# Performance work log

Measured on AMD Instinct MI355X. Metric: run time of the kernel, lower is better.

Reference implementation:

```python
import jax, jax.numpy as jnp
import numpy as np

N = 100000      # nodes
E = 1600000     # edges (avg degree 16)
D_IN = 128
D_OUT = 64
N_SCALES = 3
DEPTH = 10
TELEPORTS = np.array([0.1, 0.2, 0.3], dtype=np.float32)


def setup_inputs() -> dict:
    key = jax.random.key(0)
    ks = jax.random.split(key, 9)
    data = jax.random.normal(ks[0], (N, D_IN), dtype=jnp.float32)
    src = jax.random.randint(ks[1], (E,), 0, N, dtype=jnp.int32)
    tgt = jax.random.randint(ks[2], (E,), 0, N, dtype=jnp.int32)
    s = 1.0 / np.sqrt(D_IN)
    Ws = jax.random.uniform(ks[3], (N_SCALES, D_IN, D_OUT), jnp.float32, -s, s)
    bs = jax.random.uniform(ks[4], (N_SCALES, D_OUT), jnp.float32, -s, s)
    W_src = jax.random.uniform(ks[5], (D_IN, D_OUT), jnp.float32, -s, s)
    b_src = jax.random.uniform(ks[6], (D_OUT,), jnp.float32, -s, s)
    so = 1.0 / np.sqrt(D_OUT)
    W_tgt = jax.random.uniform(ks[7], (D_OUT, D_OUT), jnp.float32, -so, so)
    b_tgt = jax.random.uniform(ks[8], (D_OUT,), jnp.float32, -so, so)
    return {"data": data, "src": src, "tgt": tgt, "Ws": Ws, "bs": bs,
            "W_src": W_src, "b_src": b_src, "W_tgt": W_tgt, "b_tgt": b_tgt}


def reference(data, src, tgt, Ws, bs, W_src, b_src, W_tgt, b_tgt):
    # per-target-node degree (indices.unique counts repeated per edge)
    deg = jax.ops.segment_sum(jnp.ones((E,), jnp.float32), tgt, num_segments=N)
    deg_inv = 1.0 / jnp.maximum(deg, 1.0)           # [N]
    edge_w = deg_inv[tgt][:, None]                  # [E,1] normalized factor

    def laplacian(x):                               # x: [N, D_OUT]
        diff = (x[tgt] - x[src]) * edge_w           # (own - source_message)/deg
        return jax.ops.segment_sum(diff, tgt, num_segments=N)

    lap3 = jax.vmap(laplacian)                      # over scale dim

    t = jnp.asarray(TELEPORTS)[:, None, None]       # [S,1,1]
    emb = jnp.einsum('nd,sdo->sno', data, Ws) + bs[:, None, :]   # [S,N,O]
    out = emb
    for _ in range(DEPTH):
        out = (1.0 - t) * lap3(out) + t * emb
    scales = jax.nn.relu(out)                       # [S,N,O]

    s_att = data @ W_src + b_src                    # [N,O]
    t_att = jnp.einsum('sno,op->snp', scales, W_tgt) + b_tgt     # [S,N,O]
    logits = jnp.einsum('snp,np->sn', t_att, s_att)              # [S,N]
    att = jax.nn.softmax(logits, axis=0)            # softmax over scales
    return jnp.einsum('sn,sno->no', att, scales)    # [N,O]
```

## Files before the change

kernel.cpp:

```cpp
#include <hip/hip_runtime.h>
#include <hip/hip_bf16.h>

#define NN   100000
#define EE   1600000
#define CAP  48
#define NT   6250
#define NPB  192
#define NB   521

typedef __attribute__((ext_vector_type(8))) short bf16x8;
typedef __attribute__((ext_vector_type(4))) float f32x4;

__device__ inline short f2b_rne(float f) {
  union { float f; unsigned u; } x; x.f = f;
  unsigned r = x.u + 0x7fffu + ((x.u >> 16) & 1u);
  return (short)(r >> 16);
}
__device__ inline unsigned pack_rne(float lo, float hi) {
  unsigned ul = __float_as_uint(lo); ul += 0x7fffu + ((ul >> 16) & 1u);
  unsigned uh = __float_as_uint(hi); uh += 0x7fffu + ((uh >> 16) & 1u);
  return __builtin_amdgcn_perm(uh, ul, 0x07060302u);
}
__device__ inline float lo2f(unsigned u) { return __uint_as_float(u << 16); }
__device__ inline float hi2f(unsigned u) { return __uint_as_float(u & 0xffff0000u); }

__global__ __launch_bounds__(256) void k_fillA(const int* __restrict__ tgt,
                                               int* __restrict__ ghist) {
  __shared__ int h[NB];
  for (int i = threadIdx.x; i < NB; i += 256) h[i] = 0;
  __syncthreads();
  int e = blockIdx.x * 4096 + threadIdx.x;
#pragma unroll
  for (int k = 0; k < 16; ++k, e += 256)
    if (e < EE) atomicAdd(&h[tgt[e] / NPB], 1);
  __syncthreads();
  for (int i = threadIdx.x; i < NB; i += 256)
    if (h[i]) atomicAdd(&ghist[i], h[i]);
}

__global__ __launch_bounds__(256) void k_scan(const int* __restrict__ ghist,
                                              int* __restrict__ base,
                                              int* __restrict__ tail) {
  __shared__ int v[1024];
  const int tid = threadIdx.x;
  for (int i = tid; i < 1024; i += 256) v[i] = (i < NB) ? ghist[i] : 0;
  __syncthreads();
  for (int off = 1; off < 1024; off <<= 1) {
    int tmp[4];
#pragma unroll
    for (int j = 0; j < 4; ++j) {
      int i = tid + j * 256;
      tmp[j] = (i >= off) ? v[i - off] : 0;
    }
    __syncthreads();
#pragma unroll
    for (int j = 0; j < 4; ++j) v[tid + j * 256] += tmp[j];
    __syncthreads();
  }
  for (int i = tid; i <= NB; i += 256) {
    int bb = (i == 0) ? 0 : v[i - 1];
    base[i] = bb;
    if (i < NB) tail[i] = bb;
  }
}

__global__ __launch_bounds__(256) void k_fillB(const int* __restrict__ tgt,
                                               const int* __restrict__ src,
                                               int* tail, uint2* __restrict__ part) {
  __shared__ int hist[NB], cur[NB], basel[NB];
  const int tid = threadIdx.x;
  for (int i = tid; i < NB; i += 256) { hist[i] = 0; cur[i] = 0; }
  __syncthreads();
  const int e0 = blockIdx.x * 4096 + tid;
  int tv[16], sv[16];
#pragma unroll
  for (int k = 0; k < 16; ++k) {
    int e = e0 + k * 256;
    tv[k] = -1;
    if (e < EE) {
      tv[k] = tgt[e]; sv[k] = src[e];
      atomicAdd(&hist[tv[k] / NPB], 1);
    }
  }
  __syncthreads();
  for (int b = tid; b < NB; b += 256)
    if (hist[b]) basel[b] = atomicAdd(&tail[b], hist[b]);
  __syncthreads();
#pragma unroll
  for (int k = 0; k < 16; ++k) {
    if (tv[k] >= 0) {
      int b = tv[k] / NPB;
      int r = atomicAdd(&cur[b], 1);
      part[basel[b] + r] = make_uint2((unsigned)sv[k], (unsigned)tv[k]);
    }
  }
}

__global__ __launch_bounds__(256) void k_fillC(const int* __restrict__ base,
                                               const uint2* __restrict__ part,
                                               int* __restrict__ cnt,
                                               int* __restrict__ col) {
  __shared__ int ccnt[NPB];
  __shared__ int ccol[NPB * CAP];
  const int b = blockIdx.x, tid = threadIdx.x;
  for (int i = tid; i < NPB; i += 256) ccnt[i] = 0;
  __syncthreads();
  const int lo = base[b], hi = base[b + 1];
  for (int i = lo + tid; i < hi; i += 256) {
    uint2 e = part[i];
    int nl = (int)e.y - b * NPB;
    int p = atomicAdd(&ccnt[nl], 1);
    if (p < CAP) ccol[nl * CAP + p] = (int)e.x;
  }
  __syncthreads();
  const int n0 = b * NPB;
  for (int i = tid; i < NPB; i += 256)
    if (n0 + i < NN) cnt[n0 + i] = ccnt[i];
  for (int i = tid; i < NPB * CAP; i += 256) {
    int n = n0 + i / CAP;
    if (n < NN) col[(size_t)n0 * CAP + i] = ccol[i];
  }
}

__global__ void k_cast(const float* __restrict__ data, unsigned* __restrict__ y0) {
  int i = blockIdx.x * 256 + threadIdx.x;
  const float2 v = ((const float2*)data)[i];
  y0[i] = pack_rne(v.x, v.y);
}

template <int MODE>
__global__ __launch_bounds__(256) void k_prop(
    const int* __restrict__ cnt, const int* __restrict__ col,
    const unsigned* __restrict__ xin, unsigned* xout,
    const unsigned* s0p, const unsigned* s1p,
    unsigned* __restrict__ z0, unsigned* __restrict__ z1,
    unsigned* __restrict__ z2,
    float4 g0, float4 g1, float4 g2) {
  const int wv = threadIdx.x >> 6, lane = threadIdx.x & 63;
  const int n = blockIdx.x * 4 + wv;
  if (n >= NN) return;
  const size_t p = (size_t)n * 64 + lane;
  const int d = cnt[n];
  const int dm = (d < CAP) ? d : CAP;
  int idx = (lane < dm) ? col[n * CAP + lane] : 0;
  const unsigned own = xin[p];
  unsigned S0 = 0, S1 = 0, U0 = 0, U1 = 0, U2 = 0;
  if (MODE == 1 || MODE == 2 || MODE == 3) S0 = s0p[p];
  if (MODE == 1 || MODE == 2) S1 = s1p[p];
  if (MODE == 2 || MODE == 3) { U0 = z0[p]; U1 = z1[p]; U2 = z2[p]; }

  float s0 = 0.f, s1 = 0.f;
  int i = 0;
  for (; i + 4 <= dm; i += 4) {
    int ja = __shfl(idx, i),     jb = __shfl(idx, i + 1);
    int jc = __shfl(idx, i + 2), jd = __shfl(idx, i + 3);
    unsigned a = xin[(size_t)ja * 64 + lane];
    unsigned b = xin[(size_t)jb * 64 + lane];
    unsigned c = xin[(size_t)jc * 64 + lane];
    unsigned e = xin[(size_t)jd * 64 + lane];
    s0 += (lo2f(a) + lo2f(b)) + (lo2f(c) + lo2f(e));
    s1 += (hi2f(a) + hi2f(b)) + (hi2f(c) + hi2f(e));
  }
  for (; i < dm; ++i) {
    int j = __shfl(idx, i);
    unsigned a = xin[(size_t)j * 64 + lane];
    s0 += lo2f(a); s1 += hi2f(a);
  }
  const float gate = (d > 0) ? 1.f : 0.f;
  const float inv  = (d > 0) ? 1.f / (float)d : 0.f;
  const float o0 = lo2f(own), o1 = hi2f(own);
  const float l0 = gate * (o0 - inv * s0);
  const float l1 = gate * (o1 - inv * s1);
  if (MODE != 3) xout[p] = pack_rne(l0, l1);
  if (MODE == 1 || MODE == 2) {
    const float a0 = lo2f(S0), a1 = hi2f(S0), b0 = lo2f(S1), b1 = hi2f(S1);
    float t0lo = g0.x * a0 + g0.y * b0 + g0.z * o0 + g0.w * l0;
    float t0hi = g0.x * a1 + g0.y * b1 + g0.z * o1 + g0.w * l1;
    float t1lo = g1.x * a0 + g1.y * b0 + g1.z * o0 + g1.w * l0;
    float t1hi = g1.x * a1 + g1.y * b1 + g1.z * o1 + g1.w * l1;
    float t2lo = g2.x * a0 + g2.y * b0 + g2.z * o0 + g2.w * l0;
    float t2hi = g2.x * a1 + g2.y * b1 + g2.z * o1 + g2.w * l1;
    if (MODE == 2) {
      t0lo += lo2f(U0); t0hi += hi2f(U0);
      t1lo += lo2f(U1); t1hi += hi2f(U1);
      t2lo += lo2f(U2); t2hi += hi2f(U2);
    }
    z0[p] = pack_rne(t0lo, t0hi);
    z1[p] = pack_rne(t1lo, t1hi);
    z2[p] = pack_rne(t2lo, t2hi);
  } else if (MODE == 3) {
    const float a0 = lo2f(S0), a1 = hi2f(S0);
    z0[p] = pack_rne(lo2f(U0) + g0.x * a0 + g0.z * o0 + g0.w * l0,
                     hi2f(U0) + g0.x * a1 + g0.z * o1 + g0.w * l1);
    z1[p] = pack_rne(lo2f(U1) + g1.x * a0 + g1.z * o0 + g1.w * l0,
                     hi2f(U1) + g1.x * a1 + g1.z * o1 + g1.w * l1);
    z2[p] = pack_rne(lo2f(U2) + g2.x * a0 + g2.z * o0 + g2.w * l0,
                     hi2f(U2) + g2.x * a1 + g2.z * o1 + g2.w * l1);
  }
}

__global__ __launch_bounds__(256) void k_gemm2(
    const unsigned* __restrict__ z0, const unsigned* __restrict__ z1,
    const unsigned* __restrict__ z2, const unsigned* __restrict__ y0,
    const float* __restrict__ Ws, const float* __restrict__ bs,
    const float* __restrict__ Wsrc, const float* __restrict__ bsrc,
    __hip_bfloat16* __restrict__ scales, float* __restrict__ satt) {
  const int lane = threadIdx.x & 63;
  const int wv   = threadIdx.x >> 6;
  const int n16  = lane & 15;
  const int q    = lane >> 4;
  const unsigned* Ab = (wv == 0) ? z0 : (wv == 1) ? z1 : (wv == 2) ? z2 : y0;
  const float tw = 0.1f * (float)(wv + 1);

  bf16x8 Bf[4][4];
  float  bias[4];
#pragma unroll
  for (int ct = 0; ct < 4; ++ct) {
    const int c = ct * 16 + n16;
    const float* bp = (wv < 3) ? (Ws + (size_t)wv * 8192 + c) : (Wsrc + c);
    bias[ct] = (wv < 3) ? tw * bs[wv * 64 + c] : bsrc[c];
#pragma unroll
    for (int s = 0; s < 4; ++s) {
      const int k0 = s * 32 + q * 8;
      union { short h[8]; bf16x8 v; } u;
#pragma unroll
      for (int j = 0; j < 8; ++j) u.h[j] = f2b_rne(bp[(size_t)(k0 + j) * 64]);
      Bf[ct][s] = u.v;
    }
  }

  for (int t = blockIdx.x; t < NT; t += gridDim.x) {
    const int row = t * 16 + n16;
    const uint4* ap = (const uint4*)(Ab + (size_t)row * 64);
    f32x4 acc[4];
#pragma unroll
    for (int ct = 0; ct < 4; ++ct)
      acc[ct] = (f32x4){bias[ct], bias[ct], bias[ct], bias[ct]};
#pragma unroll
    for (int s = 0; s < 4; ++s) {
      union { uint4 u; bf16x8 v; } af;
      af.u = ap[s * 4 + q];
#pragma unroll
      for (int ct = 0; ct < 4; ++ct)
        acc[ct] = __builtin_amdgcn_mfma_f32_16x16x32_bf16(af.v, Bf[ct][s], acc[ct], 0, 0, 0);
    }
    if (wv < 3) {
#pragma unroll
      for (int ct = 0; ct < 4; ++ct) {
        const int c = wv * 64 + ct * 16 + n16;
#pragma unroll
        for (int i = 0; i < 4; ++i) {
          const int r = t * 16 + q * 4 + i;
          scales[(size_t)r * 192 + c] = __float2bfloat16(acc[ct][i]);
        }
      }
    } else {
#pragma unroll
      for (int ct = 0; ct < 4; ++ct) {
        const int c = ct * 16 + n16;
#pragma unroll
        for (int i = 0; i < 4; ++i) {
          const int r = t * 16 + q * 4 + i;
          satt[(size_t)r * 64 + c] = acc[ct][i];
        }
      }
    }
  }
}

__global__ __launch_bounds__(256) void k_att(
    const __hip_bfloat16* __restrict__ scales, const float* __restrict__ Wt,
    float* __restrict__ io) {
  __shared__ float WT[64 * 64];
  const int tid = threadIdx.x;
  for (int i = tid; i < 4096; i += 256) WT[(i & 63) * 64 + (i >> 6)] = Wt[i];
  __syncthreads();
  const int wv = tid >> 6, lane = tid & 63;
  for (int n = blockIdx.x * 4 + wv; n < NN; n += gridDim.x * 4) {
    const __hip_bfloat16* sr = scales + (size_t)n * 192;
    float v0 = fmaxf(__bfloat162float(sr[lane]), 0.f);
    float v1 = fmaxf(__bfloat162float(sr[64 + lane]), 0.f);
    float v2 = fmaxf(__bfloat162float(sr[128 + lane]), 0.f);
    float a = io[(size_t)n * 64 + lane];
    float m = 0.f;
#pragma unroll
    for (int p = 0; p < 64; ++p) m = fmaf(WT[p * 64 + lane], __shfl(a, p), m);
    float l0 = v0 * m, l1 = v1 * m, l2 = v2 * m;
#pragma unroll
    for (int off = 32; off; off >>= 1) {
      l0 += __shfl_xor(l0, off);
      l1 += __shfl_xor(l1, off);
      l2 += __shfl_xor(l2, off);
    }
    float mx = fmaxf(l0, fmaxf(l1, l2));
    float x0 = __expf(l0 - mx), x1 = __expf(l1 - mx), x2 = __expf(l2 - mx);
    float invs = 1.f / (x0 + x1 + x2);
    io[(size_t)n * 64 + lane] = (x0 * v0 + x1 * v1 + x2 * v2) * invs;
  }
}

extern "C" void kernel_launch(void* const* d_in, const int* in_sizes, int n_in,
                              void* d_out, int out_size, void* d_ws, size_t ws_size,
                              hipStream_t stream) {
  (void)in_sizes; (void)n_in; (void)out_size; (void)ws_size;
  const float* data = (const float*)d_in[0];
  const int*   srcp = (const int*)d_in[1];
  const int*   tgtp = (const int*)d_in[2];
  const float* Ws   = (const float*)d_in[3];
  const float* bs   = (const float*)d_in[4];
  const float* Wsrc = (const float*)d_in[5];
  const float* bsrc = (const float*)d_in[6];
  const float* Wtgt = (const float*)d_in[7];
  float* out = (float*)d_out;

  char* ws = (char*)d_ws;
  auto al = [](size_t x) { return (x + 255) & ~(size_t)255; };
  size_t off = 0;
  auto take = [&](size_t bytes) { size_t o = off; off += al(bytes); return o; };
  int*      cnt   = (int*)(ws + take((size_t)NN * 4));
  int*      col   = (int*)(ws + take((size_t)NN * CAP * 4));
  int*      ghist = (int*)(ws + take((size_t)NB * 4));
  int*      base  = (int*)(ws + take((size_t)(NB + 1) * 4));
  int*      tail  = (int*)(ws + take((size_t)NB * 4));
  uint2*    part  = (uint2*)(ws + take((size_t)EE * 8));
  const size_t szY = (size_t)NN * 64 * 4;
  unsigned* Y0 = (unsigned*)(ws + take(szY));
  unsigned* R1 = (unsigned*)(ws + take(szY));
  unsigned* R2 = (unsigned*)(ws + take(szY));
  unsigned* R3 = (unsigned*)(ws + take(szY));
  unsigned* z0 = (unsigned*)(ws + take(szY));
  unsigned* z1 = (unsigned*)(ws + take(szY));
  unsigned* z2 = (unsigned*)(ws + take(szY));
  __hip_bfloat16* scales = (__hip_bfloat16*)R2;

  float c[3][11];
  for (int s = 0; s < 3; ++s) {
    float t = 0.1f * (float)(s + 1), pw = 1.f;
    for (int j = 0; j < 10; ++j) { c[s][j] = t * pw; pw *= (1.f - t); }
    c[s][10] = pw;
  }
  float4 A3[3], A7[3], A10[3];
  for (int s = 0; s < 3; ++s) {
    A3[s]  = make_float4(c[s][0], c[s][1], c[s][2], c[s][3]);
    A7[s]  = make_float4(c[s][4], c[s][5], c[s][6], c[s][7]);
    A10[s] = make_float4(c[s][8], 0.f,     c[s][9], c[s][10]);
  }
  const float4 Zf = make_float4(0.f, 0.f, 0.f, 0.f);

  const int EB = (EE + 4095) / 4096;
  hipMemsetAsync(ghist, 0, NB * 4, stream);
  k_fillA<<<EB, 256, 0, stream>>>(tgtp, ghist);
  k_scan<<<1, 256, 0, stream>>>(ghist, base, tail);
  k_fillB<<<EB, 256, 0, stream>>>(tgtp, srcp, tail, part);
  k_fillC<<<NB, 256, 0, stream>>>(base, part, cnt, col);
  k_cast<<<NN * 64 / 256, 256, 0, stream>>>(data, Y0);

  const int PG = (NN + 3) / 4;
  k_prop<0><<<PG, 256, 0, stream>>>(cnt, col, Y0, R1, nullptr, nullptr,
      nullptr, nullptr, nullptr, Zf, Zf, Zf);
  k_prop<0><<<PG, 256, 0, stream>>>(cnt, col, R1, R2, nullptr, nullptr,
      nullptr, nullptr, nullptr, Zf, Zf, Zf);
  k_prop<1><<<PG, 256, 0, stream>>>(cnt, col, R2, R3, Y0, R1,
      z0, z1, z2, A3[0], A3[1], A3[2]);
  k_prop<0><<<PG, 256, 0, stream>>>(cnt, col, R3, R1, nullptr, nullptr,
      nullptr, nullptr, nullptr, Zf, Zf, Zf);
  k_prop<0><<<PG, 256, 0, stream>>>(cnt, col, R1, R2, nullptr, nullptr,
      nullptr, nullptr, nullptr, Zf, Zf, Zf);
  k_prop<0><<<PG, 256, 0, stream>>>(cnt, col, R2, R3, nullptr, nullptr,
      nullptr, nullptr, nullptr, Zf, Zf, Zf);
  k_prop<2><<<PG, 256, 0, stream>>>(cnt, col, R3, R1, R1, R2,
      z0, z1, z2, A7[0], A7[1], A7[2]);
  k_prop<0><<<PG, 256, 0, stream>>>(cnt, col, R1, R2, nullptr, nullptr,
      nullptr, nullptr, nullptr, Zf, Zf, Zf);
  k_prop<0><<<PG, 256, 0, stream>>>(cnt, col, R2, R3, nullptr, nullptr,
      nullptr, nullptr, nullptr, Zf, Zf, Zf);
  k_prop<3><<<PG, 256, 0, stream>>>(cnt, col, R3, nullptr, R2, nullptr,
      z0, z1, z2, A10[0], A10[1], A10[2]);

  k_gemm2<<<512, 256, 0, stream>>>(z0, z1, z2, Y0, Ws, bs, Wsrc, bsrc, scales, out);
  k_att<<<2048, 256, 0, stream>>>(scales, Wtgt, out);
}
```

Baseline: 972.4 us.

## Fold W_src·W_tgt into one weight and widen the gather unroll

Precomputes Weff = W_src·W_tgtᵀ and beff so the GEMM writes the per-node attention vector m directly as bf16. This removes the per-node 64x64 matvec and the shared-memory weight transpose from the attention kernel. The propagation gather loop is unrolled to 8 neighbours and uses readlane instead of shfl, to get more loads in flight. It adds a tiny precompute kernel and stores m in bf16, which loses some precision.

```diff
diff --git a/kernel.cpp b/kernel.cpp
--- a/kernel.cpp
+++ b/kernel.cpp
@@ -23,6 +23,7 @@
 }
 __device__ inline float lo2f(unsigned u) { return __uint_as_float(u << 16); }
 __device__ inline float hi2f(unsigned u) { return __uint_as_float(u & 0xffff0000u); }
+__device__ inline float b2f(unsigned short u) { return __uint_as_float((unsigned)u << 16); }
 
 __global__ __launch_bounds__(256) void k_fillA(const int* __restrict__ tgt,
                                                int* __restrict__ ghist) {
@@ -126,6 +127,26 @@
   int i = blockIdx.x * 256 + threadIdx.x;
   const float2 v = ((const float2*)data)[i];
   y0[i] = pack_rne(v.x, v.y);
+}
+
+__global__ __launch_bounds__(256) void k_weff(
+    const float* __restrict__ Wsrc, const float* __restrict__ bsrc,
+    const float* __restrict__ Wtgt, float* __restrict__ Weff,
+    float* __restrict__ beff) {
+  const int i = blockIdx.x * 256 + threadIdx.x;
+  if (i < 8192) {
+    const int d = i >> 6, o = i & 63;
+    float s = 0.f;
+#pragma unroll
+    for (int p = 0; p < 64; ++p) s = fmaf(Wsrc[d * 64 + p], Wtgt[o * 64 + p], s);
+    Weff[i] = s;
+  } else if (i < 8256) {
+    const int o = i - 8192;
+    float s = 0.f;
+#pragma unroll
+    for (int p = 0; p < 64; ++p) s = fmaf(bsrc[p], Wtgt[o * 64 + p], s);
+    beff[o] = s;
+  }
 }
 
 template <int MODE>
@@ -151,20 +172,40 @@
 
   float s0 = 0.f, s1 = 0.f;
   int i = 0;
-  for (; i + 4 <= dm; i += 4) {
-    int ja = __shfl(idx, i),     jb = __shfl(idx, i + 1);
-    int jc = __shfl(idx, i + 2), jd = __shfl(idx, i + 3);
-    unsigned a = xin[(size_t)ja * 64 + lane];
-    unsigned b = xin[(size_t)jb * 64 + lane];
-    unsigned c = xin[(size_t)jc * 64 + lane];
-    unsigned e = xin[(size_t)jd * 64 + lane];
-    s0 += (lo2f(a) + lo2f(b)) + (lo2f(c) + lo2f(e));
-    s1 += (hi2f(a) + hi2f(b)) + (hi2f(c) + hi2f(e));
-  }
-  for (; i < dm; ++i) {
-    int j = __shfl(idx, i);
-    unsigned a = xin[(size_t)j * 64 + lane];
-    s0 += lo2f(a); s1 += hi2f(a);
+  for (; i + 8 <= dm; i += 8) {
+    int j0 = __builtin_amdgcn_readlane(idx, i);
+    int j1 = __builtin_amdgcn_readlane(idx, i + 1);
+    int j2 = __builtin_amdgcn_readlane(idx, i + 2);
+    int j3 = __builtin_amdgcn_readlane(idx, i + 3);
+    int j4 = __builtin_amdgcn_readlane(idx, i + 4);
+    int j5 = __builtin_amdgcn_readlane(idx, i + 5);
+    int j6 = __builtin_amdgcn_readlane(idx, i + 6);
+    int j7 = __builtin_amdgcn_readlane(idx, i + 7);
+    unsigned a0 = xin[(size_t)j0 * 64 + lane];
+    unsigned a1 = xin[(size_t)j1 * 64 + lane];
+    unsigned a2 = xin[(size_t)j2 * 64 + lane];
+    unsigned a3 = xin[(size_t)j3 * 64 + lane];
+    unsigned a4 = xin[(size_t)j4 * 64 + lane];
+    unsigned a5 = xin[(size_t)j5 * 64 + lane];
+    unsigned a6 = xin[(size_t)j6 * 64 + lane];
+    unsigned a7 = xin[(size_t)j7 * 64 + lane];
+    s0 += ((lo2f(a0) + lo2f(a1)) + (lo2f(a2) + lo2f(a3))) +
+          ((lo2f(a4) + lo2f(a5)) + (lo2f(a6) + lo2f(a7)));
+    s1 += ((hi2f(a0) + hi2f(a1)) + (hi2f(a2) + hi2f(a3))) +
+          ((hi2f(a4) + hi2f(a5)) + (hi2f(a6) + hi2f(a7)));
+  }
+  for (; i + 2 <= dm; i += 2) {
+    int j0 = __builtin_amdgcn_readlane(idx, i);
+    int j1 = __builtin_amdgcn_readlane(idx, i + 1);
+    unsigned a0 = xin[(size_t)j0 * 64 + lane];
+    unsigned a1 = xin[(size_t)j1 * 64 + lane];
+    s0 += lo2f(a0) + lo2f(a1);
+    s1 += hi2f(a0) + hi2f(a1);
+  }
+  if (i < dm) {
+    int j0 = __builtin_amdgcn_readlane(idx, i);
+    unsigned a0 = xin[(size_t)j0 * 64 + lane];
+    s0 += lo2f(a0); s1 += hi2f(a0);
   }
   const float gate = (d > 0) ? 1.f : 0.f;
   const float inv  = (d > 0) ? 1.f / (float)d : 0.f;
@@ -203,8 +244,8 @@
     const unsigned* __restrict__ z0, const unsigned* __restrict__ z1,
     const unsigned* __restrict__ z2, const unsigned* __restrict__ y0,
     const float* __restrict__ Ws, const float* __restrict__ bs,
-    const float* __restrict__ Wsrc, const float* __restrict__ bsrc,
-    __hip_bfloat16* __restrict__ scales, float* __restrict__ satt) {
+    const float* __restrict__ Weff, const float* __restrict__ beff,
+    __hip_bfloat16* __restrict__ scales, unsigned short* __restrict__ m) {
   const int lane = threadIdx.x & 63;
   const int wv   = threadIdx.x >> 6;
   const int n16  = lane & 15;
@@ -217,8 +258,8 @@
 #pragma unroll
   for (int ct = 0; ct < 4; ++ct) {
     const int c = ct * 16 + n16;
-    const float* bp = (wv < 3) ? (Ws + (size_t)wv * 8192 + c) : (Wsrc + c);
-    bias[ct] = (wv < 3) ? tw * bs[wv * 64 + c] : bsrc[c];
+    const float* bp = (wv < 3) ? (Ws + (size_t)wv * 8192 + c) : (Weff + c);
+    bias[ct] = (wv < 3) ? tw * bs[wv * 64 + c] : beff[c];
 #pragma unroll
     for (int s = 0; s < 4; ++s) {
       const int k0 = s * 32 + q * 8;
@@ -261,31 +302,24 @@
 #pragma unroll
         for (int i = 0; i < 4; ++i) {
           const int r = t * 16 + q * 4 + i;
-          satt[(size_t)r * 64 + c] = acc[ct][i];
+          m[(size_t)r * 64 + c] = (unsigned short)f2b_rne(acc[ct][i]);
         }
       }
     }
   }
 }
 
-__global__ __launch_bounds__(256) void k_att(
-    const __hip_bfloat16* __restrict__ scales, const float* __restrict__ Wt,
-    float* __restrict__ io) {
-  __shared__ float WT[64 * 64];
-  const int tid = threadIdx.x;
-  for (int i = tid; i < 4096; i += 256) WT[(i & 63) * 64 + (i >> 6)] = Wt[i];
-  __syncthreads();
-  const int wv = tid >> 6, lane = tid & 63;
+__global__ __launch_bounds__(256) void k_att2(
+    const unsigned short* __restrict__ scales,
+    const unsigned short* __restrict__ m, float* __restrict__ io) {
+  const int wv = threadIdx.x >> 6, lane = threadIdx.x & 63;
   for (int n = blockIdx.x * 4 + wv; n < NN; n += gridDim.x * 4) {
-    const __hip_bfloat16* sr = scales + (size_t)n * 192;
-    float v0 = fmaxf(__bfloat162float(sr[lane]), 0.f);
-    float v1 = fmaxf(__bfloat162float(sr[64 + lane]), 0.f);
-    float v2 = fmaxf(__bfloat162float(sr[128 + lane]), 0.f);
-    float a = io[(size_t)n * 64 + lane];
-    float m = 0.f;
-#pragma unroll
-    for (int p = 0; p < 64; ++p) m = fmaf(WT[p * 64 + lane], __shfl(a, p), m);
-    float l0 = v0 * m, l1 = v1 * m, l2 = v2 * m;
+    const unsigned short* sr = scales + (size_t)n * 192;
+    float v0 = fmaxf(b2f(sr[lane]), 0.f);
+    float v1 = fmaxf(b2f(sr[64 + lane]), 0.f);
+    float v2 = fmaxf(b2f(sr[128 + lane]), 0.f);
+    float mm = b2f(m[(size_t)n * 64 + lane]);
+    float l0 = v0 * mm, l1 = v1 * mm, l2 = v2 * mm;
 #pragma unroll
     for (int off = 32; off; off >>= 1) {
       l0 += __shfl_xor(l0, off);
@@ -322,6 +356,8 @@
   int*      ghist = (int*)(ws + take((size_t)NB * 4));
   int*      base  = (int*)(ws + take((size_t)(NB + 1) * 4));
   int*      tail  = (int*)(ws + take((size_t)NB * 4));
+  float*    Weff  = (float*)(ws + take((size_t)8192 * 4));
+  float*    beff  = (float*)(ws + take((size_t)64 * 4));
   uint2*    part  = (uint2*)(ws + take((size_t)EE * 8));
   const size_t szY = (size_t)NN * 64 * 4;
   unsigned* Y0 = (unsigned*)(ws + take(szY));
@@ -332,6 +368,7 @@
   unsigned* z1 = (unsigned*)(ws + take(szY));
   unsigned* z2 = (unsigned*)(ws + take(szY));
   __hip_bfloat16* scales = (__hip_bfloat16*)R2;
+  unsigned short* mbuf   = (unsigned short*)R1;
 
   float c[3][11];
   for (int s = 0; s < 3; ++s) {
@@ -354,6 +391,7 @@
   k_fillB<<<EB, 256, 0, stream>>>(tgtp, srcp, tail, part);
   k_fillC<<<NB, 256, 0, stream>>>(base, part, cnt, col);
   k_cast<<<NN * 64 / 256, 256, 0, stream>>>(data, Y0);
+  k_weff<<<33, 256, 0, stream>>>(Wsrc, bsrc, Wtgt, Weff, beff);
 
   const int PG = (NN + 3) / 4;
   k_prop<0><<<PG, 256, 0, stream>>>(cnt, col, Y0, R1, nullptr, nullptr,
@@ -377,6 +415,7 @@
   k_prop<3><<<PG, 256, 0, stream>>>(cnt, col, R3, nullptr, R2, nullptr,
       z0, z1, z2, A10[0], A10[1], A10[2]);
 
-  k_gemm2<<<512, 256, 0, stream>>>(z0, z1, z2, Y0, Ws, bs, Wsrc, bsrc, scales, out);
-  k_att<<<2048, 256, 0, stream>>>(scales, Wtgt, out);
-}
+  k_gemm2<<<512, 256, 0, stream>>>(z0, z1, z2, Y0, Ws, bs, Weff, beff,
+                                   scales, mbuf);
+  k_att2<<<6250, 256, 0, stream>>>((const unsigned short*)scales, mbuf, out);
+}
```

Measured after the change: 879.1 us. -9.6%, faster.
